# Performance work log

Hardware: AMD Instinct MI355X
Metric: run time of the kernel (lower is better)

## Reference

```python
import jax, jax.numpy as jnp
import numpy as np

LN_EPS = 1e-5
DIM = 128
HEADS = 6
DIM_HEAD = 32
INNER = HEADS * DIM_HEAD          # 192
FF_INNER = int(DIM * 4 * 2 / 3)   # 341 (GEGLU inner dim)
LOCAL_WINDOW = 200
CACHE = 3
COMPRESS = 2
TW = LOCAL_WINDOW + CACHE         # 203
B = 2
T = 12800                         # 32 chunks of 400


def layer_norm(x, w, b):
    m = x.mean(-1, keepdims=True)
    v = ((x - m) ** 2).mean(-1, keepdims=True)
    return (x - m) / jnp.sqrt(v + LN_EPS) * w + b


def apply_rotary(q, k):
    # q, k: (b, h, n, d); standard half-rotation rotary over absolute positions
    d = q.shape[-1]
    n = q.shape[2]
    inv_freq = 1.0 / (10000.0 ** (jnp.arange(0, d, 2, dtype=jnp.float32) / d))
    freqs = jnp.arange(n, dtype=jnp.float32)[:, None] * inv_freq  # (n, d/2)
    emb = jnp.concatenate([freqs, freqs], axis=-1)                # (n, d)
    cos = jnp.cos(emb).astype(q.dtype)
    sin = jnp.sin(emb).astype(q.dtype)

    def rot_half(x):
        x1, x2 = jnp.split(x, 2, axis=-1)
        return jnp.concatenate([-x2, x1], axis=-1)

    rope = lambda x: x * cos + rot_half(x) * sin
    return rope(q), rope(k)


def local_attention(q, k, v, w):
    # causal local attention, look_backward=1 window, look_forward=0 (lucidrains LocalAttention)
    b, h, n, d = q.shape
    nw = n // w
    q, k = apply_rotary(q, k)
    qw = q.reshape(b, h, nw, w, d)

    def look_around(x):
        xw = x.reshape(b, h, nw, w, d)
        prev = jnp.pad(xw[:, :, :-1], ((0, 0), (0, 0), (1, 0), (0, 0), (0, 0)))
        return jnp.concatenate([prev, xw], axis=3)  # (b,h,nw,2w,d)

    kw = look_around(k)
    vw = look_around(v)

    t = jnp.arange(n).reshape(nw, w)
    tk_prev = jnp.pad(t[:-1], ((1, 0), (0, 0)), constant_values=-1)
    tk = jnp.concatenate([tk_prev, t], axis=1)  # (nw, 2w); -1 marks padding
    mask = (t[:, :, None] >= tk[:, None, :]) & (tk[:, None, :] >= 0)  # (nw, w, 2w)

    sim = jnp.einsum('bhwid,bhwjd->bhwij', qw, kw) * (d ** -0.5)
    neg = jnp.finfo(sim.dtype).min
    sim = jnp.where(mask[None, None], sim, neg)
    attn = jax.nn.softmax(sim, axis=-1)
    out = jnp.einsum('bhwij,bhwjd->bhwid', attn, vw)
    return out.reshape(b, h, n, d)


def local_mha(x, ln_w, ln_b, wqkv, wo, window):
    h = layer_norm(x, ln_w, ln_b)
    qkv = h @ wqkv                       # (b, n, 3*INNER)
    q, k, v = jnp.split(qkv, 3, axis=-1)

    def split_heads(t):
        bb, n, _ = t.shape
        return t.reshape(bb, n, HEADS, DIM_HEAD).transpose(0, 2, 1, 3)

    out = local_attention(split_heads(q), split_heads(k), split_heads(v), window)
    bb, hh, n, d = out.shape
    out = out.transpose(0, 2, 1, 3).reshape(bb, n, hh * d)
    return out @ wo


def feed_forward(x, ln_w, ln_b, w1, w2):
    h = layer_norm(x, ln_w, ln_b) @ w1   # (b, n, 2*FF_INNER)
    a, gate = jnp.split(h, 2, axis=-1)
    return (a * jax.nn.gelu(gate, approximate=False)) @ w2


def local_trans(x, ln1_w, ln1_b, wqkv, wo, ln2_w, ln2_b, w1, w2, window):
    n_layers = ln1_w.shape[0]
    for i in range(n_layers):
        x = x + local_mha(x, ln1_w[i], ln1_b[i], wqkv[i], wo[i], window)
        x = x + feed_forward(x, ln2_w[i], ln2_b[i], w1[i], w2[i])
    return x


def setup_inputs() -> dict:
    key = jax.random.key(0)
    ks = jax.random.split(key, 16)
    std = 0.02
    rn = lambda k, shape: jax.random.normal(k, shape, dtype=jnp.float32) * std
    inp = {
        'x': jax.random.normal(ks[0], (B, DIM, T), dtype=jnp.float32),
        'cache_token': jax.random.normal(ks[1], (1, CACHE * COMPRESS, DIM), dtype=jnp.float32),
    }
    ki = 2
    for g in ('dt', 'lt'):
        inp[g + '_ln1_w'] = jnp.ones((2, DIM), jnp.float32)
        inp[g + '_ln1_b'] = jnp.zeros((2, DIM), jnp.float32)
        inp[g + '_wqkv'] = rn(ks[ki], (2, DIM, 3 * INNER)); ki += 1
        inp[g + '_wo'] = rn(ks[ki], (2, INNER, DIM)); ki += 1
        inp[g + '_ln2_w'] = jnp.ones((2, DIM), jnp.float32)
        inp[g + '_ln2_b'] = jnp.zeros((2, DIM), jnp.float32)
        inp[g + '_w1'] = rn(ks[ki], (2, DIM, 2 * FF_INNER)); ki += 1
        inp[g + '_w2'] = rn(ks[ki], (2, FF_INNER, DIM)); ki += 1
    inp['conv_w'] = rn(ks[ki], (DIM, DIM, COMPRESS)); ki += 1
    inp['conv_b'] = jnp.zeros((DIM,), jnp.float32)
    return inp


def reference(x, cache_token,
              dt_ln1_w, dt_ln1_b, dt_wqkv, dt_wo, dt_ln2_w, dt_ln2_b, dt_w1, dt_w2,
              lt_ln1_w, lt_ln1_b, lt_wqkv, lt_wo, lt_ln2_w, lt_ln2_b, lt_w1, lt_w2,
              conv_w, conv_b):
    feat = x.transpose(0, 2, 1)                     # (B, T, C)
    b, t, c = feat.shape
    chunk = LOCAL_WINDOW * COMPRESS                 # 400
    nchunks = t // chunk
    feat = feat.reshape(b, nchunks, chunk, c)
    ct = jnp.broadcast_to(cache_token[:, None], (b, nchunks, CACHE * COMPRESS, c))
    feat = jnp.concatenate([ct, feat], axis=2)      # interleave cache tokens per chunk
    feat = feat.reshape(b, nchunks * (chunk + CACHE * COMPRESS), c)

    # DownTrans: 2-layer local transformer (window 406) + strided conv compress
    feat = local_trans(feat, dt_ln1_w, dt_ln1_b, dt_wqkv, dt_wo,
                       dt_ln2_w, dt_ln2_b, dt_w1, dt_w2, TW * COMPRESS)
    y = jax.lax.conv_general_dilated(
        feat.transpose(0, 2, 1), conv_w, (COMPRESS,), 'VALID',
        dimension_numbers=('NCH', 'OIH', 'NCH')) + conv_b[None, :, None]
    feat = y.transpose(0, 2, 1)                     # (B, n/2, C)

    # remaining depth-2 local transformer (window 203)
    feat = local_trans(feat, lt_ln1_w, lt_ln1_b, lt_wqkv, lt_wo,
                       lt_ln2_w, lt_ln2_b, lt_w1, lt_w2, TW)
    return feat
```

## Files before the change

kernel.cpp:

```cpp
#include <hip/hip_runtime.h>
#include <cstdint>
#include <cstddef>

#define DIM    128
#define HEADS  6
#define INNER  192
#define QKV3   576
#define FFI    341
#define FF2    682
#define GGP    352
#define BATCH  2
#define T_IN   12800
#define N1     12992
#define N2     6496
#define ROWS1  (BATCH * N1)
#define ROWS2  (BATCH * N2)
#define W_DT   406
#define W_LT   203

typedef unsigned short ushortT;
typedef unsigned int u32;
typedef __bf16 bf16x8 __attribute__((ext_vector_type(8)));
typedef float f32x4 __attribute__((ext_vector_type(4)));

__device__ __forceinline__ f32x4 mfma16(bf16x8 a, bf16x8 b, f32x4 c) {
  return __builtin_amdgcn_mfma_f32_16x16x32_bf16(a, b, c, 0, 0, 0);
}
__device__ __forceinline__ ushortT f2bf(float x) {
  union { __bf16 b; ushortT u; } c; c.b = (__bf16)x; return c.u;
}
__device__ __forceinline__ void async_copy16(const ushortT* g, ushortT* l) {
  __builtin_amdgcn_global_load_lds(
      (const __attribute__((address_space(1))) unsigned int*)g,
      (__attribute__((address_space(3))) unsigned int*)l, 16, 0, 0);
}

static constexpr size_t OF_FEAT = 0;
static constexpr size_t OF_H    = OF_FEAT + (size_t)ROWS1 * DIM;
static constexpr size_t OF_QKH  = OF_H + (size_t)ROWS1 * DIM / 2;
static constexpr size_t SZ_QKH  = ((size_t)(ROWS1 + 128) * 384) / 2;
static constexpr size_t OF_AO   = OF_QKH + SZ_QKH;
static constexpr size_t OF_VT   = OF_AO + (size_t)ROWS1 * INNER / 2;
static constexpr size_t SZ_VT   = ((size_t)384 * (N1 + 128)) / 2;
static constexpr size_t OF_GG   = OF_VT + SZ_VT;
static constexpr size_t OF_F2   = OF_GG + (size_t)ROWS1 * GGP / 2;
static constexpr size_t OF_WT   = OF_F2 + (size_t)ROWS2 * DIM;
static constexpr size_t WT_QKV = 0;
static constexpr size_t WT_WO  = 81920;
static constexpr size_t WT_W1  = 106496;
static constexpr size_t WT_W2  = 204800;
static constexpr size_t WT_SET = 249856;
static constexpr size_t OF_CW  = OF_WT + (4 * WT_SET) / 2 + 64;

__global__ void build_feat_kernel(const float* __restrict__ x,
                                  const float* __restrict__ cache,
                                  float* __restrict__ feat) {
  int idx = blockIdx.x * 256 + threadIdx.x;
  if (idx >= ROWS1 * DIM) return;
  int d = idx & 127;
  int row = idx >> 7;
  int b = row / N1;
  int i = row - b * N1;
  int c = i / 406;
  int j = i - c * 406;
  float v;
  if (j < 6) v = cache[j * DIM + d];
  else       v = x[((size_t)b * DIM + d) * T_IN + (c * 400 + j - 6)];
  feat[idx] = v;
}

__global__ __launch_bounds__(256) void ln_kernel(const float* __restrict__ x,
                                                 ushortT* __restrict__ y,
                                                 const float* __restrict__ w,
                                                 const float* __restrict__ bb,
                                                 int rows) {
  int row = blockIdx.x * 4 + (threadIdx.x >> 6);
  if (row >= rows) return;
  int lane = threadIdx.x & 63;
  const float* xr = x + (size_t)row * DIM;
  float2 v = *(const float2*)(xr + lane * 2);
  float s = v.x + v.y;
#pragma unroll
  for (int off = 32; off; off >>= 1) s += __shfl_xor(s, off);
  float mean = s * (1.0f / 128.0f);
  float dx = v.x - mean, dy = v.y - mean;
  float q = dx * dx + dy * dy;
#pragma unroll
  for (int off = 32; off; off >>= 1) q += __shfl_xor(q, off);
  float rstd = rsqrtf(q * (1.0f / 128.0f) + 1e-5f);
  float2 wv = *(const float2*)(w + lane * 2);
  float2 bv = *(const float2*)(bb + lane * 2);
  u32 packed = (u32)f2bf(dx * rstd * wv.x + bv.x) |
               ((u32)f2bf(dy * rstd * wv.y + bv.y) << 16);
  *(u32*)(y + (size_t)row * DIM + lane * 2) = packed;
}

__global__ __launch_bounds__(256) void gemm_bf16(
    const ushortT* __restrict__ A, int lda,
    const ushortT* __restrict__ Wt, int ldw,
    const float* __restrict__ C, float* __restrict__ Co, int ldc,
    int M, int N, int Kpad, int addC) {
  __shared__ ushortT As[128 * 32];
  __shared__ ushortT Bs[128 * 32];
  const int tid = threadIdx.x;
  const int wid = tid >> 6, lane = tid & 63;
  const int ck = lane & 15, quad = lane >> 4;
  const int bm = blockIdx.y * 128, bn = blockIdx.x * 128;
  const int wr = (wid >> 1) * 64, wc = (wid & 1) * 64;
  f32x4 acc[4][4];
#pragma unroll
  for (int t = 0; t < 4; t++)
#pragma unroll
    for (int u = 0; u < 4; u++) acc[t][u] = (f32x4){0.f, 0.f, 0.f, 0.f};

  for (int k0 = 0; k0 < Kpad; k0 += 32) {
    __syncthreads();
#pragma unroll
    for (int c2 = 0; c2 < 2; c2++) {
      int idx = c2 * 256 + wid * 64 + lane;
      int row = idx >> 2, seg = (idx & 3) << 3;
      int ar = bm + row; if (ar > M - 1) ar = M - 1;
      async_copy16(A + (size_t)ar * lda + k0 + seg, As + (size_t)(c2 * 256 + wid * 64) * 8);
      async_copy16(Wt + (size_t)(bn + row) * ldw + k0 + seg, Bs + (size_t)(c2 * 256 + wid * 64) * 8);
    }
    __syncthreads();
    bf16x8 af[4], bfr[4];
#pragma unroll
    for (int t = 0; t < 4; t++)
      af[t] = *(const bf16x8*)&As[(wr + t * 16 + ck) * 32 + quad * 8];
#pragma unroll
    for (int u = 0; u < 4; u++)
      bfr[u] = *(const bf16x8*)&Bs[(wc + u * 16 + ck) * 32 + quad * 8];
#pragma unroll
    for (int t = 0; t < 4; t++)
#pragma unroll
      for (int u = 0; u < 4; u++)
        acc[t][u] = mfma16(af[t], bfr[u], acc[t][u]);
  }

#pragma unroll
  for (int t = 0; t < 4; t++) {
#pragma unroll
    for (int r = 0; r < 4; r++) {
      int row = bm + wr + t * 16 + quad * 4 + r;
      if (row >= M) continue;
      const float* crow = C + (size_t)row * ldc;
      float* orow = Co + (size_t)row * ldc;
#pragma unroll
      for (int u = 0; u < 4; u++) {
        int col = bn + wc + u * 16 + ck;
        if (col < N) {
          float v = acc[t][u][r];
          if (addC) v += crow[col];
          orow[col] = v;
        }
      }
    }
  }
}

__global__ __launch_bounds__(256) void gemm_bf16_64(
    const ushortT* __restrict__ A, int lda,
    const ushortT* __restrict__ Wt, int ldw,
    const float* __restrict__ C, float* __restrict__ Co, int ldc,
    int M, int N, int Kpad, int addC) {
  __shared__ ushortT As[64 * 32];
  __shared__ ushortT Bs[128 * 32];
  const int tid = threadIdx.x;
  const int wid = tid >> 6, lane = tid & 63;
  const int ck = lane & 15, quad = lane >> 4;
  const int bm = blockIdx.y * 64, bn = blockIdx.x * 128;
  const int wr = (wid >> 1) * 32, wc = (wid & 1) * 64;
  f32x4 acc[2][4];
#pragma unroll
  for (int t = 0; t < 2; t++)
#pragma unroll
    for (int u = 0; u < 4; u++) acc[t][u] = (f32x4){0.f, 0.f, 0.f, 0.f};

  for (int k0 = 0; k0 < Kpad; k0 += 32) {
    __syncthreads();
    {
      int idx = wid * 64 + lane;
      int row = idx >> 2, seg = (idx & 3) << 3;
      int ar = bm + row; if (ar > M - 1) ar = M - 1;
      async_copy16(A + (size_t)ar * lda + k0 + seg, As + (size_t)(wid * 64) * 8);
    }
#pragma unroll
    for (int c2 = 0; c2 < 2; c2++) {
      int idx = c2 * 256 + wid * 64 + lane;
      int row = idx >> 2, seg = (idx & 3) << 3;
      async_copy16(Wt + (size_t)(bn + row) * ldw + k0 + seg, Bs + (size_t)(c2 * 256 + wid * 64) * 8);
    }
    __syncthreads();
    bf16x8 af[2], bfr[4];
#pragma unroll
    for (int t = 0; t < 2; t++)
      af[t] = *(const bf16x8*)&As[(wr + t * 16 + ck) * 32 + quad * 8];
#pragma unroll
    for (int u = 0; u < 4; u++)
      bfr[u] = *(const bf16x8*)&Bs[(wc + u * 16 + ck) * 32 + quad * 8];
#pragma unroll
    for (int t = 0; t < 2; t++)
#pragma unroll
      for (int u = 0; u < 4; u++)
        acc[t][u] = mfma16(af[t], bfr[u], acc[t][u]);
  }

#pragma unroll
  for (int t = 0; t < 2; t++) {
#pragma unroll
    for (int r = 0; r < 4; r++) {
      int row = bm + wr + t * 16 + quad * 4 + r;
      if (row >= M) continue;
      const float* crow = C + (size_t)row * ldc;
      float* orow = Co + (size_t)row * ldc;
#pragma unroll
      for (int u = 0; u < 4; u++) {
        int col = bn + wc + u * 16 + ck;
        if (col < N) {
          float v = acc[t][u][r];
          if (addC) v += crow[col];
          orow[col] = v;
        }
      }
    }
  }
}

__global__ __launch_bounds__(256) void gemm_qkv(
    const ushortT* __restrict__ A,
    const ushortT* __restrict__ Wt,
    ushortT* __restrict__ qkh,
    ushortT* __restrict__ vt,
    int M, int nseq, int nseqP) {
  __shared__ ushortT As[128 * 32];
  __shared__ ushortT Bs[128 * 32];
  const int tid = threadIdx.x;
  const int wid = tid >> 6, lane = tid & 63;
  const int ck = lane & 15, quad = lane >> 4;
  const int bm = blockIdx.y * 128, bn = blockIdx.x * 128;
  const int wr = (wid >> 1) * 64, wc = (wid & 1) * 64;
  f32x4 acc[4][4];
#pragma unroll
  for (int t = 0; t < 4; t++)
#pragma unroll
    for (int u = 0; u < 4; u++) acc[t][u] = (f32x4){0.f, 0.f, 0.f, 0.f};

  for (int k0 = 0; k0 < 128; k0 += 32) {
    __syncthreads();
#pragma unroll
    for (int c2 = 0; c2 < 2; c2++) {
      int idx = c2 * 256 + wid * 64 + lane;
      int row = idx >> 2, seg = (idx & 3) << 3;
      int ar = bm + row; if (ar > M - 1) ar = M - 1;
      async_copy16(A + (size_t)ar * 128 + k0 + seg, As + (size_t)(c2 * 256 + wid * 64) * 8);
      async_copy16(Wt + (size_t)(bn + row) * 128 + k0 + seg, Bs + (size_t)(c2 * 256 + wid * 64) * 8);
    }
    __syncthreads();
    bf16x8 af[4], bfr[4];
#pragma unroll
    for (int t = 0; t < 4; t++)
      af[t] = *(const bf16x8*)&As[(wr + t * 16 + ck) * 32 + quad * 8];
#pragma unroll
    for (int u = 0; u < 4; u++)
      bfr[u] = *(const bf16x8*)&Bs[(wc + u * 16 + ck) * 32 + quad * 8];
#pragma unroll
    for (int t = 0; t < 4; t++)
#pragma unroll
      for (int u = 0; u < 4; u++)
        acc[t][u] = mfma16(af[t], bfr[u], acc[t][u]);
  }

  const int s = bn + wc;
  if (s >= QKV3) return;

  if (s < 384) {
    const bool isQ = s < 192;
    const float SCq = 0.17677669529663687f * 1.4426950408889634f;
    const float invf = 1.0f / powf(10000.0f, (float)ck * (1.0f / 16.0f));
#pragma unroll
    for (int t = 0; t < 4; t++) {
#pragma unroll
      for (int r = 0; r < 4; r++) {
        int row = bm + wr + t * 16 + quad * 4 + r;
        if (row >= M) continue;
        int pos = (row >= nseq) ? row - nseq : row;
        float sn, cs;
        sincosf((float)pos * invf, &sn, &cs);
        ushortT* orow = qkh + (size_t)row * 384;
#pragma unroll
        for (int u = 0; u < 4; u += 2) {
          float a0 = acc[t][u][r], a1 = acc[t][u + 1][r];
          float o0 = a0 * cs - a1 * sn;
          float o1 = a1 * cs + a0 * sn;
          if (isQ) { o0 *= SCq; o1 *= SCq; }
          int c0 = s + u * 16 + ck;
          orow[c0]      = f2bf(o0);
          orow[c0 + 16] = f2bf(o1);
        }
      }
    }
  } else {
#pragma unroll
    for (int t = 0; t < 4; t++) {
      int rowb = bm + wr + t * 16 + quad * 4;
      if (rowb >= M) continue;
      int bb = (rowb >= nseq) ? 1 : 0;
      int posb = rowb - bb * nseq;
#pragma unroll
      for (int u = 0; u < 4; u++) {
        int cv = s - 384 + u * 16 + ck;
        int hh = cv >> 5, d = cv & 31;
        ushort4 o;
        o.x = f2bf(acc[t][u][0]);
        o.y = f2bf(acc[t][u][1]);
        o.z = f2bf(acc[t][u][2]);
        o.w = f2bf(acc[t][u][3]);
        *(ushort4*)(vt + ((size_t)((bb * 6 + hh) * 32 + d)) * nseqP + posb) = o;
      }
    }
  }
}

__global__ __launch_bounds__(256) void gemm_w1g(
    const ushortT* __restrict__ A,
    const ushortT* __restrict__ Wt,
    ushortT* __restrict__ gg,
    int M) {
  __shared__ ushortT As[128 * 32];
  __shared__ ushortT Bs[128 * 32];
  const int tid = threadIdx.x;
  const int wid = tid >> 6, lane = tid & 63;
  const int ck = lane & 15, quad = lane >> 4;
  const int bm = blockIdx.y * 128, bn = blockIdx.x * 128;
  const int wr = (wid >> 1) * 64, wc = (wid & 1) * 64;
  f32x4 acc[4][4];
#pragma unroll
  for (int t = 0; t < 4; t++)
#pragma unroll
    for (int u = 0; u < 4; u++) acc[t][u] = (f32x4){0.f, 0.f, 0.f, 0.f};

  for (int k0 = 0; k0 < 128; k0 += 32) {
    __syncthreads();
#pragma unroll
    for (int c2 = 0; c2 < 2; c2++) {
      int idx = c2 * 256 + wid * 64 + lane;
      int row = idx >> 2, seg = (idx & 3) << 3;
      int ar = bm + row; if (ar > M - 1) ar = M - 1;
      async_copy16(A + (size_t)ar * 128 + k0 + seg, As + (size_t)(c2 * 256 + wid * 64) * 8);
      async_copy16(Wt + (size_t)(bn + row) * 128 + k0 + seg, Bs + (size_t)(c2 * 256 + wid * 64) * 8);
    }
    __syncthreads();
    bf16x8 af[4], bfr[4];
#pragma unroll
    for (int t = 0; t < 4; t++)
      af[t] = *(const bf16x8*)&As[(wr + t * 16 + ck) * 32 + quad * 8];
#pragma unroll
    for (int u = 0; u < 4; u++)
      bfr[u] = *(const bf16x8*)&Bs[(wc + u * 16 + ck) * 32 + quad * 8];
#pragma unroll
    for (int t = 0; t < 4; t++)
#pragma unroll
      for (int u = 0; u < 4; u++)
        acc[t][u] = mfma16(af[t], bfr[u], acc[t][u]);
  }

  const int s = bn + wc;
  if (s >= 704) return;
#pragma unroll
  for (int t = 0; t < 4; t++) {
#pragma unroll
    for (int r = 0; r < 4; r++) {
      int row = bm + wr + t * 16 + quad * 4 + r;
      if (row >= M) continue;
      ushortT* orow = gg + (size_t)row * GGP;
#pragma unroll
      for (int u = 0; u < 4; u += 2) {
        float a  = acc[t][u][r];
        float gt = acc[t][u + 1][r];
        float ge = 0.5f * gt * (1.0f + erff(gt * 0.70710678118654752f));
        int p = ((s + u * 16) >> 5) * 16 + ck;
        orow[p] = f2bf(a * ge);
      }
    }
  }
}

__global__ __launch_bounds__(256) void gemm_f32(
    const float* __restrict__ A, int lda,
    const float* __restrict__ W, int ldw,
    float* __restrict__ C, int ldc,
    int M, int N, int K, int addC, const float* __restrict__ bias) {
  __shared__ float As[16][68];
  __shared__ float Ws[16][68];
  int tid = threadIdx.x;
  int bm = blockIdx.y * 64, bn = blockIdx.x * 64;
  int tx = tid & 15, ty = tid >> 4;
  float acc[4][4] = {{0.f,0.f,0.f,0.f},{0.f,0.f,0.f,0.f},{0.f,0.f,0.f,0.f},{0.f,0.f,0.f,0.f}};
  int arow = tid >> 2;
  int akq = (tid & 3) << 2;
  int wk = tid >> 4;
  int wn = (tid & 15) << 2;
  for (int k0 = 0; k0 < K; k0 += 16) {
    float4 av = *(const float4*)(A + (size_t)(bm + arow) * lda + k0 + akq);
    float4 wv = *(const float4*)(W + (size_t)(k0 + wk) * ldw + bn + wn);
    __syncthreads();
    As[akq + 0][arow] = av.x; As[akq + 1][arow] = av.y;
    As[akq + 2][arow] = av.z; As[akq + 3][arow] = av.w;
    *(float4*)&Ws[wk][wn] = wv;
    __syncthreads();
#pragma unroll
    for (int kk = 0; kk < 16; kk++) {
      float4 a4 = *(const float4*)&As[kk][ty << 2];
      float4 b4 = *(const float4*)&Ws[kk][tx << 2];
      float aa[4] = {a4.x, a4.y, a4.z, a4.w};
      float bv2[4] = {b4.x, b4.y, b4.z, b4.w};
#pragma unroll
      for (int i = 0; i < 4; i++)
#pragma unroll
        for (int j = 0; j < 4; j++)
          acc[i][j] = fmaf(aa[i], bv2[j], acc[i][j]);
    }
  }
#pragma unroll
  for (int i = 0; i < 4; i++) {
    int row = bm + (ty << 2) + i;
    float* crow = C + (size_t)row * ldc;
#pragma unroll
    for (int j = 0; j < 4; j++) {
      int col = bn + (tx << 2) + j;
      float v = acc[i][j];
      if (bias) v += bias[col];
      if (addC) v += crow[col];
      crow[col] = v;
    }
  }
}

__global__ __launch_bounds__(256) void attn_kernel(
    const ushortT* __restrict__ qkh, const ushortT* __restrict__ vt,
    ushortT* __restrict__ out, int nseq, int nseqP, int w, int qgroups) {
  __shared__ ushortT Ks[128 * 40];
  __shared__ ushortT Vs[32 * 136];
  __shared__ ushortT Ps[4 * 16 * 72];

  const int bx = blockIdx.x;
  const int c = bx / qgroups;
  const int g = bx - c * qgroups;
  const int h = blockIdx.y;
  const int b = blockIdx.z;
  const int tid = threadIdx.x;
  const int wv = tid >> 6;
  const int lane = tid & 63;
  const int ck = lane & 15;
  const int quad = lane >> 4;

  const ushortT* gq = qkh + (size_t)b * nseq * 384;
  const ushortT* gv = vt + ((size_t)(b * 6 + h) * 32) * nseqP;
  const int cw = c * w;
  const int q0 = g * 64;
  const int qt = q0 + wv * 16;
  const bool wave_on = qt < w;

  const int j0 = (c > 0) ? (c - 1) * w : 0;
  const int jend_block = cw + min(q0 + 63, w - 1) + 1;
  const int jend_wave = wave_on ? (cw + min(qt + 15, w - 1) + 1) : 0;

  bf16x8 qf;
  {
    int qrow = cw + min(qt + ck, w - 1);
    qf = *(const bf16x8*)(gq + (size_t)qrow * 384 + h * 32 + quad * 8);
  }

  f32x4 olo = {0.f, 0.f, 0.f, 0.f};
  f32x4 ohi = {0.f, 0.f, 0.f, 0.f};
  float lp[4] = {0.f, 0.f, 0.f, 0.f};
  ushortT* pw = Ps + wv * 16 * 72;

  for (int tb = j0; tb < jend_block; tb += 128) {
    __syncthreads();
    for (int i = tid; i < 512; i += 256) {
      int row = i >> 2, dg = (i & 3) << 3;
      *(float4*)&Ks[row * 40 + dg] =
          *(const float4*)(gq + (size_t)(tb + row) * 384 + 192 + h * 32 + dg);
    }
    for (int i = tid; i < 512; i += 256) {
      int d = i >> 4, kg = (i & 15) << 3;
      *(float4*)&Vs[d * 136 + kg] = *(const float4*)(gv + (size_t)d * nseqP + tb + kg);
    }
    __syncthreads();

    const int glim = min(128, jend_wave - tb);
    for (int g64 = 0; g64 < glim; g64 += 64) {
      int r0 = g64 + 2 * ck;
      bf16x8 kf0 = *(const bf16x8*)&Ks[(r0) * 40 + quad * 8];
      bf16x8 kf1 = *(const bf16x8*)&Ks[(r0 + 1) * 40 + quad * 8];
      bf16x8 kf2 = *(const bf16x8*)&Ks[(r0 + 32) * 40 + quad * 8];
      bf16x8 kf3 = *(const bf16x8*)&Ks[(r0 + 33) * 40 + quad * 8];
      f32x4 z = {0.f, 0.f, 0.f, 0.f};
      f32x4 s0 = mfma16(qf, kf0, z);
      f32x4 s1 = mfma16(qf, kf1, z);
      f32x4 s2 = mfma16(qf, kf2, z);
      f32x4 s3 = mfma16(qf, kf3, z);
      if (tb + g64 + 63 > cw + qt) {
        int key0 = tb + g64 + 2 * ck;
#pragma unroll
        for (int r = 0; r < 4; r++) {
          int qg = cw + qt + quad * 4 + r;
          if (key0 > qg)      s0[r] = -__builtin_inff();
          if (key0 + 1 > qg)  s1[r] = -__builtin_inff();
          if (key0 + 32 > qg) s2[r] = -__builtin_inff();
          if (key0 + 33 > qg) s3[r] = -__builtin_inff();
        }
      }
#pragma unroll
      for (int r = 0; r < 4; r++) {
        float p0 = exp2f(s0[r]);
        float p1 = exp2f(s1[r]);
        float p2 = exp2f(s2[r]);
        float p3 = exp2f(s3[r]);
        lp[r] += (p0 + p1) + (p2 + p3);
        int row72 = (quad * 4 + r) * 72;
        *(u32*)&pw[row72 + 2 * ck]      = (u32)f2bf(p0) | ((u32)f2bf(p1) << 16);
        *(u32*)&pw[row72 + 32 + 2 * ck] = (u32)f2bf(p2) | ((u32)f2bf(p3) << 16);
      }
      bf16x8 pf0 = *(const bf16x8*)&pw[ck * 72 + quad * 8];
      bf16x8 pf1 = *(const bf16x8*)&pw[ck * 72 + 32 + quad * 8];
      bf16x8 vlo0 = *(const bf16x8*)&Vs[ck * 136 + g64 + quad * 8];
      bf16x8 vhi0 = *(const bf16x8*)&Vs[(ck + 16) * 136 + g64 + quad * 8];
      bf16x8 vlo1 = *(const bf16x8*)&Vs[ck * 136 + g64 + 32 + quad * 8];
      bf16x8 vhi1 = *(const bf16x8*)&Vs[(ck + 16) * 136 + g64 + 32 + quad * 8];
      olo = mfma16(pf0, vlo0, olo);
      olo = mfma16(pf1, vlo1, olo);
      ohi = mfma16(pf0, vhi0, ohi);
      ohi = mfma16(pf1, vhi1, ohi);
    }
  }

  if (wave_on) {
#pragma unroll
    for (int r = 0; r < 4; r++) {
      float lr = lp[r];
      lr += __shfl_xor(lr, 1);
      lr += __shfl_xor(lr, 2);
      lr += __shfl_xor(lr, 4);
      lr += __shfl_xor(lr, 8);
      int qi = qt + quad * 4 + r;
      if (qi < w) {
        float inv = 1.0f / lr;
        ushortT* orow = out + ((size_t)b * nseq + cw + qi) * INNER + h * 32;
        orow[ck]      = f2bf(olo[r] * inv);
        orow[ck + 16] = f2bf(ohi[r] * inv);
      }
    }
  }
}

__global__ void wconvert_all_kernel(
    const float* __restrict__ dq, const float* __restrict__ dwo,
    const float* __restrict__ dw1, const float* __restrict__ dw2,
    const float* __restrict__ lq, const float* __restrict__ lwo,
    const float* __restrict__ lw1, const float* __restrict__ lw2,
    const float* __restrict__ convw,
    ushortT* __restrict__ wt, float* __restrict__ cwout) {
  int idx = blockIdx.x * 256 + threadIdx.x;
  const int TOTW = 4 * (int)WT_SET;
  if (idx < TOTW) {
    int s = idx / (int)WT_SET;
    int rem = idx - s * (int)WT_SET;
    int lyr = s & 1;
    const float* Wq = ((s < 2) ? dq : lq) + (size_t)lyr * DIM * QKV3;
    const float* Wo = ((s < 2) ? dwo : lwo) + (size_t)lyr * INNER * DIM;
    const float* W1 = ((s < 2) ? dw1 : lw1) + (size_t)lyr * DIM * FF2;
    const float* W2 = ((s < 2) ? dw2 : lw2) + (size_t)lyr * FFI * DIM;
    float v = 0.f;
    if (rem < (int)WT_WO) {
      int n = rem >> 7, k = rem & 127;
      if (n < QKV3) v = Wq[(size_t)k * QKV3 + n];
    } else if (rem < (int)WT_W1) {
      int r = rem - (int)WT_WO;
      int n = r / INNER, k = r - n * INNER;
      v = Wo[(size_t)k * DIM + n];
    } else if (rem < (int)WT_W2) {
      int r = rem - (int)WT_W1;
      int n = r >> 7, k = r & 127;
      if (n < 704) {
        int blk = n >> 5, wi = n & 31;
        int p = blk * 16 + (wi & 15);
        if (p < FFI) {
          int src = (wi < 16) ? p : FFI + p;
          v = W1[(size_t)k * FF2 + src];
        }
      }
    } else {
      int r = rem - (int)WT_W2;
      int n = r / GGP, k = r - n * GGP;
      if (k < FFI) v = W2[(size_t)k * DIM + n];
    }
    wt[idx] = f2bf(v);
  } else {
    int r = idx - TOTW;
    if (r < 256 * DIM) {
      int kidx = r >> 7, o = r & 127;
      int kk = kidx >> 7, i = kidx & 127;
      cwout[r] = convw[((size_t)o * DIM + i) * 2 + kk];
    }
  }
}

static void run_layer(float* F, float* Fout, ushortT* h, ushortT* qkh, ushortT* vtb,
                      ushortT* attnb, ushortT* ggb, const ushortT* wt,
                      int M, int nseq, int w,
                      const float* ln1w, const float* ln1b,
                      const float* ln2w, const float* ln2b,
                      hipStream_t stream) {
  int lnBlocks = (M + 3) / 4;
  int nseqP = nseq + 128;
  int gy = (M + 127) / 128;
  int gy64 = (M + 63) / 64;
  ln_kernel<<<lnBlocks, 256, 0, stream>>>(F, h, ln1w, ln1b, M);
  gemm_qkv<<<dim3(5, gy), 256, 0, stream>>>(h, wt + WT_QKV, qkh, vtb, M, nseq, nseqP);
  int nw = nseq / w;
  int qgroups = (w + 63) / 64;
  attn_kernel<<<dim3(nw * qgroups, HEADS, BATCH), 256, 0, stream>>>(qkh, vtb, attnb,
                                                                    nseq, nseqP, w, qgroups);
  gemm_bf16_64<<<dim3(1, gy64), 256, 0, stream>>>(attnb, INNER, wt + WT_WO, INNER, F, F, DIM,
                                                  M, DIM, INNER, 1);
  ln_kernel<<<lnBlocks, 256, 0, stream>>>(F, h, ln2w, ln2b, M);
  gemm_w1g<<<dim3(6, gy), 256, 0, stream>>>(h, wt + WT_W1, ggb, M);
  gemm_bf16_64<<<dim3(1, gy64), 256, 0, stream>>>(ggb, GGP, wt + WT_W2, GGP, F, Fout, DIM,
                                                  M, DIM, GGP, 1);
}

extern "C" void kernel_launch(void* const* d_in, const int* in_sizes, int n_in,
                              void* d_out, int out_size, void* d_ws, size_t ws_size,
                              hipStream_t stream) {
  const float* x        = (const float*)d_in[0];
  const float* cache    = (const float*)d_in[1];
  const float* dt_ln1_w = (const float*)d_in[2];
  const float* dt_ln1_b = (const float*)d_in[3];
  const float* dt_wqkv  = (const float*)d_in[4];
  const float* dt_wo    = (const float*)d_in[5];
  const float* dt_ln2_w = (const float*)d_in[6];
  const float* dt_ln2_b = (const float*)d_in[7];
  const float* dt_w1    = (const float*)d_in[8];
  const float* dt_w2    = (const float*)d_in[9];
  const float* lt_ln1_w = (const float*)d_in[10];
  const float* lt_ln1_b = (const float*)d_in[11];
  const float* lt_wqkv  = (const float*)d_in[12];
  const float* lt_wo    = (const float*)d_in[13];
  const float* lt_ln2_w = (const float*)d_in[14];
  const float* lt_ln2_b = (const float*)d_in[15];
  const float* lt_w1    = (const float*)d_in[16];
  const float* lt_w2    = (const float*)d_in[17];
  const float* conv_w   = (const float*)d_in[18];
  const float* conv_b   = (const float*)d_in[19];

  float* ws     = (float*)d_ws;
  float* feat   = ws + OF_FEAT;
  ushortT* h    = (ushortT*)(ws + OF_H);
  ushortT* qkh  = (ushortT*)(ws + OF_QKH);
  ushortT* attnb= (ushortT*)(ws + OF_AO);
  ushortT* vtb  = (ushortT*)(ws + OF_VT);
  ushortT* ggb  = (ushortT*)(ws + OF_GG);
  float* feat2  = ws + OF_F2;
  ushortT* wt   = (ushortT*)(ws + OF_WT);
  float* cw     = ws + OF_CW;
  float* outf   = (float*)d_out;

  {
    int total = 4 * (int)WT_SET + 256 * DIM;
    wconvert_all_kernel<<<(total + 255) / 256, 256, 0, stream>>>(
        dt_wqkv, dt_wo, dt_w1, dt_w2, lt_wqkv, lt_wo, lt_w1, lt_w2,
        conv_w, wt, cw);
  }

  build_feat_kernel<<<(ROWS1 * DIM + 255) / 256, 256, 0, stream>>>(x, cache, feat);

  for (int lyr = 0; lyr < 2; lyr++) {
    run_layer(feat, feat, h, qkh, vtb, attnb, ggb, wt + lyr * WT_SET,
              ROWS1, N1, W_DT,
              dt_ln1_w + lyr * DIM, dt_ln1_b + lyr * DIM,
              dt_ln2_w + lyr * DIM, dt_ln2_b + lyr * DIM, stream);
  }

  gemm_f32<<<dim3(DIM / 64, ROWS2 / 64), 256, 0, stream>>>(feat, 256, cw, DIM, feat2, DIM,
                                                           ROWS2, DIM, 256, 0, conv_b);

  for (int lyr = 0; lyr < 2; lyr++) {
    float* Fo = (lyr == 1) ? outf : feat2;
    run_layer(feat2, Fo, h, qkh, vtb, attnb, ggb, wt + (2 + lyr) * WT_SET,
              ROWS2, N2, W_LT,
              lt_ln1_w + lyr * DIM, lt_ln1_b + lyr * DIM,
              lt_ln2_w + lyr * DIM, lt_ln2_b + lyr * DIM, stream);
  }
}
```

Measured before the change: 620.2 us.

## Fuse following LayerNorm into residual output-projection GEMM epilogues

The Wo and W2 GEMM epilogues now compute the LayerNorm of the updated residual rows and write the bf16 normalized activations directly. Row sums and sums of squares are reduced with shuffles and shared memory across the two column halves. This removes the separate ln_kernel launches inside each layer, along with their re-read of the fp32 residual. Variance is now computed as E[x^2]-mean^2, which is less numerically stable, and the M%64 bounds checks are dropped on the assumption that M is a multiple of 64.

Result: faster. 598.0 us (-3.6%).

```diff
diff --git a/kernel.cpp b/kernel.cpp
--- a/kernel.cpp
+++ b/kernel.cpp
@@ -95,132 +95,116 @@
   *(u32*)(y + (size_t)row * DIM + lane * 2) = packed;
 }
 
-__global__ __launch_bounds__(256) void gemm_bf16(
+__global__ __launch_bounds__(256) void gemm_nln(
     const ushortT* __restrict__ A, int lda,
     const ushortT* __restrict__ Wt, int ldw,
-    const float* __restrict__ C, float* __restrict__ Co, int ldc,
-    int M, int N, int Kpad, int addC) {
-  __shared__ ushortT As[128 * 32];
+    const float* __restrict__ C, float* __restrict__ Co,
+    int M, int Kpad, int addC,
+    const float* __restrict__ lnw, const float* __restrict__ lnb,
+    ushortT* __restrict__ hout) {
+  __shared__ ushortT As[64 * 32];
   __shared__ ushortT Bs[128 * 32];
+  __shared__ float lnS[64][4];
   const int tid = threadIdx.x;
   const int wid = tid >> 6, lane = tid & 63;
   const int ck = lane & 15, quad = lane >> 4;
-  const int bm = blockIdx.y * 128, bn = blockIdx.x * 128;
-  const int wr = (wid >> 1) * 64, wc = (wid & 1) * 64;
-  f32x4 acc[4][4];
-#pragma unroll
-  for (int t = 0; t < 4; t++)
+  const int bm = blockIdx.y * 64;
+  const int wr = (wid >> 1) * 32, wc = (wid & 1) * 64;
+  const int half = wid & 1;
+  f32x4 acc[2][4];
+#pragma unroll
+  for (int t = 0; t < 2; t++)
 #pragma unroll
     for (int u = 0; u < 4; u++) acc[t][u] = (f32x4){0.f, 0.f, 0.f, 0.f};
 
   for (int k0 = 0; k0 < Kpad; k0 += 32) {
     __syncthreads();
+    {
+      int idx = wid * 64 + lane;
+      int row = idx >> 2, seg = (idx & 3) << 3;
+      async_copy16(A + (size_t)(bm + row) * lda + k0 + seg, As + (size_t)(wid * 64) * 8);
+    }
 #pragma unroll
     for (int c2 = 0; c2 < 2; c2++) {
       int idx = c2 * 256 + wid * 64 + lane;
       int row = idx >> 2, seg = (idx & 3) << 3;
-      int ar = bm + row; if (ar > M - 1) ar = M - 1;
-      async_copy16(A + (size_t)ar * lda + k0 + seg, As + (size_t)(c2 * 256 + wid * 64) * 8);
-      async_copy16(Wt + (size_t)(bn + row) * ldw + k0 + seg, Bs + (size_t)(c2 * 256 + wid * 64) * 8);
-    }
-    __syncthreads();
-    bf16x8 af[4], bfr[4];
-#pragma unroll
-    for (int t = 0; t < 4; t++)
+      async_copy16(Wt + (size_t)row * ldw + k0 + seg, Bs + (size_t)(c2 * 256 + wid * 64) * 8);
+    }
+    __syncthreads();
+    bf16x8 af[2], bfr[4];
+#pragma unroll
+    for (int t = 0; t < 2; t++)
       af[t] = *(const bf16x8*)&As[(wr + t * 16 + ck) * 32 + quad * 8];
 #pragma unroll
     for (int u = 0; u < 4; u++)
       bfr[u] = *(const bf16x8*)&Bs[(wc + u * 16 + ck) * 32 + quad * 8];
 #pragma unroll
-    for (int t = 0; t < 4; t++)
+    for (int t = 0; t < 2; t++)
 #pragma unroll
       for (int u = 0; u < 4; u++)
         acc[t][u] = mfma16(af[t], bfr[u], acc[t][u]);
   }
 
-#pragma unroll
-  for (int t = 0; t < 4; t++) {
+  float res[2][4][4];
+#pragma unroll
+  for (int t = 0; t < 2; t++) {
 #pragma unroll
     for (int r = 0; r < 4; r++) {
       int row = bm + wr + t * 16 + quad * 4 + r;
-      if (row >= M) continue;
-      const float* crow = C + (size_t)row * ldc;
-      float* orow = Co + (size_t)row * ldc;
+      const float* crow = C + (size_t)row * DIM;
+      float* orow = Co + (size_t)row * DIM;
 #pragma unroll
       for (int u = 0; u < 4; u++) {
-        int col = bn + wc + u * 16 + ck;
-        if (col < N) {
-          float v = acc[t][u][r];
-          if (addC) v += crow[col];
-          orow[col] = v;
+        int col = wc + u * 16 + ck;
+        float v = acc[t][u][r];
+        if (addC) v += crow[col];
+        res[t][r][u] = v;
+        orow[col] = v;
+      }
+    }
+  }
+
+  if (hout) {
+#pragma unroll
+    for (int t = 0; t < 2; t++) {
+#pragma unroll
+      for (int r = 0; r < 4; r++) {
+        float s1 = ((res[t][r][0] + res[t][r][1]) + (res[t][r][2] + res[t][r][3]));
+        float s2 = ((res[t][r][0] * res[t][r][0] + res[t][r][1] * res[t][r][1]) +
+                    (res[t][r][2] * res[t][r][2] + res[t][r][3] * res[t][r][3]));
+        s1 += __shfl_xor(s1, 1); s2 += __shfl_xor(s2, 1);
+        s1 += __shfl_xor(s1, 2); s2 += __shfl_xor(s2, 2);
+        s1 += __shfl_xor(s1, 4); s2 += __shfl_xor(s2, 4);
+        s1 += __shfl_xor(s1, 8); s2 += __shfl_xor(s2, 8);
+        if (ck == 0) {
+          int rowIn = wr + t * 16 + quad * 4 + r;
+          lnS[rowIn][half * 2]     = s1;
+          lnS[rowIn][half * 2 + 1] = s2;
         }
       }
     }
-  }
-}
-
-__global__ __launch_bounds__(256) void gemm_bf16_64(
-    const ushortT* __restrict__ A, int lda,
-    const ushortT* __restrict__ Wt, int ldw,
-    const float* __restrict__ C, float* __restrict__ Co, int ldc,
-    int M, int N, int Kpad, int addC) {
-  __shared__ ushortT As[64 * 32];
-  __shared__ ushortT Bs[128 * 32];
-  const int tid = threadIdx.x;
-  const int wid = tid >> 6, lane = tid & 63;
-  const int ck = lane & 15, quad = lane >> 4;
-  const int bm = blockIdx.y * 64, bn = blockIdx.x * 128;
-  const int wr = (wid >> 1) * 32, wc = (wid & 1) * 64;
-  f32x4 acc[2][4];
-#pragma unroll
-  for (int t = 0; t < 2; t++)
-#pragma unroll
-    for (int u = 0; u < 4; u++) acc[t][u] = (f32x4){0.f, 0.f, 0.f, 0.f};
-
-  for (int k0 = 0; k0 < Kpad; k0 += 32) {
-    __syncthreads();
-    {
-      int idx = wid * 64 + lane;
-      int row = idx >> 2, seg = (idx & 3) << 3;
-      int ar = bm + row; if (ar > M - 1) ar = M - 1;
-      async_copy16(A + (size_t)ar * lda + k0 + seg, As + (size_t)(wid * 64) * 8);
-    }
-#pragma unroll
-    for (int c2 = 0; c2 < 2; c2++) {
-      int idx = c2 * 256 + wid * 64 + lane;
-      int row = idx >> 2, seg = (idx & 3) << 3;
-      async_copy16(Wt + (size_t)(bn + row) * ldw + k0 + seg, Bs + (size_t)(c2 * 256 + wid * 64) * 8);
-    }
-    __syncthreads();
-    bf16x8 af[2], bfr[4];
-#pragma unroll
-    for (int t = 0; t < 2; t++)
-      af[t] = *(const bf16x8*)&As[(wr + t * 16 + ck) * 32 + quad * 8];
-#pragma unroll
-    for (int u = 0; u < 4; u++)
-      bfr[u] = *(const bf16x8*)&Bs[(wc + u * 16 + ck) * 32 + quad * 8];
-#pragma unroll
-    for (int t = 0; t < 2; t++)
-#pragma unroll
-      for (int u = 0; u < 4; u++)
-        acc[t][u] = mfma16(af[t], bfr[u], acc[t][u]);
-  }
-
-#pragma unroll
-  for (int t = 0; t < 2; t++) {
-#pragma unroll
-    for (int r = 0; r < 4; r++) {
-      int row = bm + wr + t * 16 + quad * 4 + r;
-      if (row >= M) continue;
-      const float* crow = C + (size_t)row * ldc;
-      float* orow = Co + (size_t)row * ldc;
-#pragma unroll
-      for (int u = 0; u < 4; u++) {
-        int col = bn + wc + u * 16 + ck;
-        if (col < N) {
-          float v = acc[t][u][r];
-          if (addC) v += crow[col];
-          orow[col] = v;
+    __syncthreads();
+    float lw[4], lb[4];
+#pragma unroll
+    for (int u = 0; u < 4; u++) {
+      lw[u] = lnw[wc + u * 16 + ck];
+      lb[u] = lnb[wc + u * 16 + ck];
+    }
+#pragma unroll
+    for (int t = 0; t < 2; t++) {
+#pragma unroll
+      for (int r = 0; r < 4; r++) {
+        int rowIn = wr + t * 16 + quad * 4 + r;
+        float S1 = lnS[rowIn][0] + lnS[rowIn][2];
+        float S2 = lnS[rowIn][1] + lnS[rowIn][3];
+        float mean = S1 * (1.0f / 128.0f);
+        float var = S2 * (1.0f / 128.0f) - mean * mean;
+        float rstd = rsqrtf(var + 1e-5f);
+        ushortT* hrow = hout + (size_t)(bm + rowIn) * DIM;
+#pragma unroll
+        for (int u = 0; u < 4; u++) {
+          int col = wc + u * 16 + ck;
+          hrow[col] = f2bf((res[t][r][u] - mean) * rstd * lw[u] + lb[u]);
         }
       }
     }
@@ -611,25 +595,23 @@
 static void run_layer(float* F, float* Fout, ushortT* h, ushortT* qkh, ushortT* vtb,
                       ushortT* attnb, ushortT* ggb, const ushortT* wt,
                       int M, int nseq, int w,
-                      const float* ln1w, const float* ln1b,
                       const float* ln2w, const float* ln2b,
+                      const float* nlnw, const float* nlnb,
                       hipStream_t stream) {
-  int lnBlocks = (M + 3) / 4;
   int nseqP = nseq + 128;
   int gy = (M + 127) / 128;
-  int gy64 = (M + 63) / 64;
-  ln_kernel<<<lnBlocks, 256, 0, stream>>>(F, h, ln1w, ln1b, M);
+  int gy64 = M / 64;
   gemm_qkv<<<dim3(5, gy), 256, 0, stream>>>(h, wt + WT_QKV, qkh, vtb, M, nseq, nseqP);
   int nw = nseq / w;
   int qgroups = (w + 63) / 64;
   attn_kernel<<<dim3(nw * qgroups, HEADS, BATCH), 256, 0, stream>>>(qkh, vtb, attnb,
                                                                     nseq, nseqP, w, qgroups);
-  gemm_bf16_64<<<dim3(1, gy64), 256, 0, stream>>>(attnb, INNER, wt + WT_WO, INNER, F, F, DIM,
-                                                  M, DIM, INNER, 1);
-  ln_kernel<<<lnBlocks, 256, 0, stream>>>(F, h, ln2w, ln2b, M);
+  gemm_nln<<<dim3(1, gy64), 256, 0, stream>>>(attnb, INNER, wt + WT_WO, INNER, F, F,
+                                              M, INNER, 1, ln2w, ln2b, h);
   gemm_w1g<<<dim3(6, gy), 256, 0, stream>>>(h, wt + WT_W1, ggb, M);
-  gemm_bf16_64<<<dim3(1, gy64), 256, 0, stream>>>(ggb, GGP, wt + WT_W2, GGP, F, Fout, DIM,
-                                                  M, DIM, GGP, 1);
+  gemm_nln<<<dim3(1, gy64), 256, 0, stream>>>(ggb, GGP, wt + WT_W2, GGP, F, Fout,
+                                              M, GGP, 1, nlnw, nlnb,
+                                              nlnw ? h : (ushortT*)nullptr);
 }
 
 extern "C" void kernel_launch(void* const* d_in, const int* in_sizes, int n_in,
@@ -676,22 +658,23 @@
   }
 
   build_feat_kernel<<<(ROWS1 * DIM + 255) / 256, 256, 0, stream>>>(x, cache, feat);
-
-  for (int lyr = 0; lyr < 2; lyr++) {
-    run_layer(feat, feat, h, qkh, vtb, attnb, ggb, wt + lyr * WT_SET,
-              ROWS1, N1, W_DT,
-              dt_ln1_w + lyr * DIM, dt_ln1_b + lyr * DIM,
-              dt_ln2_w + lyr * DIM, dt_ln2_b + lyr * DIM, stream);
-  }
+  ln_kernel<<<ROWS1 / 4, 256, 0, stream>>>(feat, h, dt_ln1_w, dt_ln1_b, ROWS1);
+
+  run_layer(feat, feat, h, qkh, vtb, attnb, ggb, wt + 0 * WT_SET,
+            ROWS1, N1, W_DT,
+            dt_ln2_w, dt_ln2_b, dt_ln1_w + DIM, dt_ln1_b + DIM, stream);
+  run_layer(feat, feat, h, qkh, vtb, attnb, ggb, wt + 1 * WT_SET,
+            ROWS1, N1, W_DT,
+            dt_ln2_w + DIM, dt_ln2_b + DIM, nullptr, nullptr, stream);
 
   gemm_f32<<<dim3(DIM / 64, ROWS2 / 64), 256, 0, stream>>>(feat, 256, cw, DIM, feat2, DIM,
                                                            ROWS2, DIM, 256, 0, conv_b);
-
-  for (int lyr = 0; lyr < 2; lyr++) {
-    float* Fo = (lyr == 1) ? outf : feat2;
-    run_layer(feat2, Fo, h, qkh, vtb, attnb, ggb, wt + (2 + lyr) * WT_SET,
-              ROWS2, N2, W_LT,
-              lt_ln1_w + lyr * DIM, lt_ln1_b + lyr * DIM,
-              lt_ln2_w + lyr * DIM, lt_ln2_b + lyr * DIM, stream);
-  }
-}
+  ln_kernel<<<ROWS2 / 4, 256, 0, stream>>>(feat2, h, lt_ln1_w, lt_ln1_b, ROWS2);
+
+  run_layer(feat2, feat2, h, qkh, vtb, attnb, ggb, wt + 2 * WT_SET,
+            ROWS2, N2, W_LT,
+            lt_ln2_w, lt_ln2_b, lt_ln1_w + DIM, lt_ln1_b + DIM, stream);
+  run_layer(feat2, outf, h, qkh, vtb, attnb, ggb, wt + 3 * WT_SET,
+            ROWS2, N2, W_LT,
+            lt_ln2_w + DIM, lt_ln2_b + DIM, nullptr, nullptr, stream);
+}
```
